# Kernel optimization log

Measured on AMD Instinct MI355X. Metric: run time of the kernel, lower is better.

## Reference

```python
import jax, jax.numpy as jnp
import numpy as np

NBINS = 256  # skimage threshold_otsu default


def _otsu_threshold(x):
    """Global Otsu threshold over the whole array, matching skimage.filters.threshold_otsu."""
    counts, edges = jnp.histogram(x.reshape(-1), bins=NBINS)
    counts = counts.astype(jnp.float32)
    centers = 0.5 * (edges[:-1] + edges[1:])  # [NBINS]

    # class probabilities / weights for all candidate thresholds
    w1 = jnp.cumsum(counts)                       # weight of class <= t
    w2 = jnp.cumsum(counts[::-1])[::-1]           # weight of class > t
    csum = jnp.cumsum(counts * centers)
    csum_rev = jnp.cumsum((counts * centers)[::-1])[::-1]
    m1 = csum / jnp.maximum(w1, 1.0)              # class means (guard empty bins)
    m2 = csum_rev / jnp.maximum(w2, 1.0)

    # between-class variance at each split point
    var12 = w1[:-1] * w2[1:] * (m1[:-1] - m2[1:]) ** 2  # [NBINS-1]
    idx = jnp.argmax(var12)
    return centers[idx]


def setup_inputs() -> dict:
    key = jax.random.key(0)
    inputs = jax.random.normal(key, (16, 1024, 2048, 1), dtype=jnp.float32)
    return {"inputs": inputs}


def reference(inputs) -> jnp.ndarray:
    x = inputs.astype(jnp.float32)
    thresh = _otsu_threshold(x)
    # ((image > thresh) * 1).astype(float32)
    return (x > thresh).astype(jnp.float32)
```

## Files before the change

kernel.cpp:

```cpp
#include <hip/hip_runtime.h>
#include <stdint.h>

#define NBINS 256
#define NCOPY 32

__device__ __forceinline__ uint32_t f2mono(float f) {
    uint32_t u = __float_as_uint(f);
    return (u & 0x80000000u) ? ~u : (u | 0x80000000u);
}
__device__ __forceinline__ float mono2f(uint32_t u) {
    uint32_t b = (u & 0x80000000u) ? (u & 0x7FFFFFFFu) : ~u;
    return __uint_as_float(b);
}

__device__ __forceinline__ float edge_at(int i, float minv, float delta) {
    return __fadd_rn(__fmul_rn((float)i, delta), minv);
}

__global__ void k_init(uint32_t* ws) {
    int i = threadIdx.x;
    if (i == 0) ws[0] = 0xFFFFFFFFu;
    if (i == 1) ws[1] = 0u;
    if (i == 2) ws[2] = 0u;
    if (i >= 4 && i < 4 + NBINS) ws[i] = 0u;
}

__device__ __forceinline__ float min4(float4 v) {
    return fminf(fminf(v.x, v.y), fminf(v.z, v.w));
}
__device__ __forceinline__ float max4(float4 v) {
    return fmaxf(fmaxf(v.x, v.y), fmaxf(v.z, v.w));
}

__global__ void __launch_bounds__(256) k_minmax(const float* __restrict__ in,
                                                int n, uint32_t* ws) {
    int tid = blockIdx.x * blockDim.x + threadIdx.x;
    int stride = gridDim.x * blockDim.x;
    int n4 = n >> 2;
    const float4* in4 = (const float4*)in;
    float vmin = INFINITY, vmax = -INFINITY;

    int i = tid;
    for (; i + 7 * stride < n4; i += 8 * stride) {
        float4 v0 = in4[i];
        float4 v1 = in4[i + stride];
        float4 v2 = in4[i + 2 * stride];
        float4 v3 = in4[i + 3 * stride];
        float4 v4 = in4[i + 4 * stride];
        float4 v5 = in4[i + 5 * stride];
        float4 v6 = in4[i + 6 * stride];
        float4 v7 = in4[i + 7 * stride];
        float mn0 = fminf(fminf(min4(v0), min4(v1)), fminf(min4(v2), min4(v3)));
        float mn1 = fminf(fminf(min4(v4), min4(v5)), fminf(min4(v6), min4(v7)));
        float mx0 = fmaxf(fmaxf(max4(v0), max4(v1)), fmaxf(max4(v2), max4(v3)));
        float mx1 = fmaxf(fmaxf(max4(v4), max4(v5)), fmaxf(max4(v6), max4(v7)));
        vmin = fminf(vmin, fminf(mn0, mn1));
        vmax = fmaxf(vmax, fmaxf(mx0, mx1));
    }
    for (; i < n4; i += stride) {
        float4 v = in4[i];
        vmin = fminf(vmin, min4(v));
        vmax = fmaxf(vmax, max4(v));
    }
    for (int j = (n4 << 2) + tid; j < n; j += stride) {
        float v = in[j];
        vmin = fminf(vmin, v);
        vmax = fmaxf(vmax, v);
    }
#pragma unroll
    for (int off = 32; off > 0; off >>= 1) {
        vmin = fminf(vmin, __shfl_down(vmin, off));
        vmax = fmaxf(vmax, __shfl_down(vmax, off));
    }
    __shared__ float smin[4], smax[4];
    int wave = threadIdx.x >> 6, lane = threadIdx.x & 63;
    if (lane == 0) { smin[wave] = vmin; smax[wave] = vmax; }
    __syncthreads();
    if (threadIdx.x == 0) {
        float m = smin[0], M = smax[0];
        for (int w = 1; w < 4; ++w) { m = fminf(m, smin[w]); M = fmaxf(M, smax[w]); }
        atomicMin(&ws[0], f2mono(m));
        atomicMax(&ws[1], f2mono(M));
    }
}

__device__ __forceinline__ int bin_of(float v, float minv, float invd) {
    float t = (v - minv) * invd;
    t = fminf(fmaxf(t, 0.0f), 255.0f);
    return (int)t;
}

__global__ void __launch_bounds__(256) k_hist(const float* __restrict__ in,
                                              int n, uint32_t* ws) {
    __shared__ uint32_t h[NBINS * NCOPY];
    for (int i = threadIdx.x; i < NBINS * NCOPY; i += blockDim.x) h[i] = 0;
    __syncthreads();
    float minv = mono2f(ws[0]);
    float maxv = mono2f(ws[1]);
    float invd = __fdiv_rn(256.0f, __fsub_rn(maxv, minv));
    int c = threadIdx.x & (NCOPY - 1);

    int tid = blockIdx.x * blockDim.x + threadIdx.x;
    int stride = gridDim.x * blockDim.x;
    int n4 = n >> 2;
    const float4* in4 = (const float4*)in;
    int i = tid;
    for (; i + 3 * stride < n4; i += 4 * stride) {
        float4 q0 = in4[i];
        float4 q1 = in4[i + stride];
        float4 q2 = in4[i + 2 * stride];
        float4 q3 = in4[i + 3 * stride];
        atomicAdd(&h[bin_of(q0.x, minv, invd) * NCOPY + c], 1u);
        atomicAdd(&h[bin_of(q0.y, minv, invd) * NCOPY + c], 1u);
        atomicAdd(&h[bin_of(q0.z, minv, invd) * NCOPY + c], 1u);
        atomicAdd(&h[bin_of(q0.w, minv, invd) * NCOPY + c], 1u);
        atomicAdd(&h[bin_of(q1.x, minv, invd) * NCOPY + c], 1u);
        atomicAdd(&h[bin_of(q1.y, minv, invd) * NCOPY + c], 1u);
        atomicAdd(&h[bin_of(q1.z, minv, invd) * NCOPY + c], 1u);
        atomicAdd(&h[bin_of(q1.w, minv, invd) * NCOPY + c], 1u);
        atomicAdd(&h[bin_of(q2.x, minv, invd) * NCOPY + c], 1u);
        atomicAdd(&h[bin_of(q2.y, minv, invd) * NCOPY + c], 1u);
        atomicAdd(&h[bin_of(q2.z, minv, invd) * NCOPY + c], 1u);
        atomicAdd(&h[bin_of(q2.w, minv, invd) * NCOPY + c], 1u);
        atomicAdd(&h[bin_of(q3.x, minv, invd) * NCOPY + c], 1u);
        atomicAdd(&h[bin_of(q3.y, minv, invd) * NCOPY + c], 1u);
        atomicAdd(&h[bin_of(q3.z, minv, invd) * NCOPY + c], 1u);
        atomicAdd(&h[bin_of(q3.w, minv, invd) * NCOPY + c], 1u);
    }
    for (; i < n4; i += stride) {
        float4 q = in4[i];
        atomicAdd(&h[bin_of(q.x, minv, invd) * NCOPY + c], 1u);
        atomicAdd(&h[bin_of(q.y, minv, invd) * NCOPY + c], 1u);
        atomicAdd(&h[bin_of(q.z, minv, invd) * NCOPY + c], 1u);
        atomicAdd(&h[bin_of(q.w, minv, invd) * NCOPY + c], 1u);
    }
    for (int j = (n4 << 2) + tid; j < n; j += stride) {
        atomicAdd(&h[bin_of(in[j], minv, invd) * NCOPY + c], 1u);
    }
    __syncthreads();
    for (int b = threadIdx.x; b < NBINS; b += blockDim.x) {
        uint32_t s = 0;
#pragma unroll
        for (int k = 0; k < NCOPY; ++k) s += h[b * NCOPY + k];
        if (s) atomicAdd(&ws[4 + b], s);
    }
}

__global__ void k_otsu(uint32_t* ws) {
    __shared__ float cnt[NBINS], ctr[NBINS], w1[NBINS], w2[NBINS],
                     cs[NBINS], csr[NBINS], scan[NBINS];
    int i = threadIdx.x;
    float minv = mono2f(ws[0]);
    float maxv = mono2f(ws[1]);
    float delta = __fdiv_rn(__fsub_rn(maxv, minv), 256.0f);

    cnt[i] = (float)ws[4 + i];
    float e0 = edge_at(i, minv, delta);
    float e1 = edge_at(i + 1, minv, delta);
    ctr[i] = __fmul_rn(0.5f, __fadd_rn(e0, e1));
    __syncthreads();

    scan[i] = cnt[i]; __syncthreads();
    for (int off = 1; off < NBINS; off <<= 1) {
        float v = scan[i];
        if (i >= off) v = __fadd_rn(scan[i - off], v);
        __syncthreads(); scan[i] = v; __syncthreads();
    }
    w1[i] = scan[i]; __syncthreads();

    scan[i] = __fmul_rn(cnt[i], ctr[i]); __syncthreads();
    for (int off = 1; off < NBINS; off <<= 1) {
        float v = scan[i];
        if (i >= off) v = __fadd_rn(scan[i - off], v);
        __syncthreads(); scan[i] = v; __syncthreads();
    }
    cs[i] = scan[i]; __syncthreads();

    scan[i] = cnt[i]; __syncthreads();
    for (int off = 1; off < NBINS; off <<= 1) {
        float v = scan[i];
        if (i + off < NBINS) v = __fadd_rn(v, scan[i + off]);
        __syncthreads(); scan[i] = v; __syncthreads();
    }
    w2[i] = scan[i]; __syncthreads();

    scan[i] = __fmul_rn(cnt[i], ctr[i]); __syncthreads();
    for (int off = 1; off < NBINS; off <<= 1) {
        float v = scan[i];
        if (i + off < NBINS) v = __fadd_rn(v, scan[i + off]);
        __syncthreads(); scan[i] = v; __syncthreads();
    }
    csr[i] = scan[i]; __syncthreads();

    if (i < NBINS - 1) {
        float m1 = __fdiv_rn(cs[i], fmaxf(w1[i], 1.0f));
        float m2 = __fdiv_rn(csr[i + 1], fmaxf(w2[i + 1], 1.0f));
        float d = __fsub_rn(m1, m2);
        float sq = __fmul_rn(d, d);
        scan[i] = __fmul_rn(__fmul_rn(w1[i], w2[i + 1]), sq);
    }
    __syncthreads();
    if (i == 0) {
        int best = 0; float bv = scan[0];
        for (int k = 1; k < NBINS - 1; ++k) {
            float v = scan[k];
            if (v > bv) { bv = v; best = k; }
        }
        ws[2] = __float_as_uint(ctr[best]);
    }
}

__global__ void __launch_bounds__(256) k_bin(const float* __restrict__ in,
                                             float* __restrict__ out,
                                             int n, const uint32_t* __restrict__ ws) {
    float t = __uint_as_float(ws[2]);
    int tid = blockIdx.x * blockDim.x + threadIdx.x;
    int stride = gridDim.x * blockDim.x;
    int n4 = n >> 2;
    const float4* in4 = (const float4*)in;
    float4* out4 = (float4*)out;
    int i = tid;
    for (; i + 3 * stride < n4; i += 4 * stride) {
        float4 v0 = in4[i];
        float4 v1 = in4[i + stride];
        float4 v2 = in4[i + 2 * stride];
        float4 v3 = in4[i + 3 * stride];
        float4 r0, r1, r2, r3;
        r0.x = v0.x > t ? 1.0f : 0.0f; r0.y = v0.y > t ? 1.0f : 0.0f;
        r0.z = v0.z > t ? 1.0f : 0.0f; r0.w = v0.w > t ? 1.0f : 0.0f;
        r1.x = v1.x > t ? 1.0f : 0.0f; r1.y = v1.y > t ? 1.0f : 0.0f;
        r1.z = v1.z > t ? 1.0f : 0.0f; r1.w = v1.w > t ? 1.0f : 0.0f;
        r2.x = v2.x > t ? 1.0f : 0.0f; r2.y = v2.y > t ? 1.0f : 0.0f;
        r2.z = v2.z > t ? 1.0f : 0.0f; r2.w = v2.w > t ? 1.0f : 0.0f;
        r3.x = v3.x > t ? 1.0f : 0.0f; r3.y = v3.y > t ? 1.0f : 0.0f;
        r3.z = v3.z > t ? 1.0f : 0.0f; r3.w = v3.w > t ? 1.0f : 0.0f;
        out4[i] = r0;
        out4[i + stride] = r1;
        out4[i + 2 * stride] = r2;
        out4[i + 3 * stride] = r3;
    }
    for (; i < n4; i += stride) {
        float4 v = in4[i];
        float4 r;
        r.x = v.x > t ? 1.0f : 0.0f;
        r.y = v.y > t ? 1.0f : 0.0f;
        r.z = v.z > t ? 1.0f : 0.0f;
        r.w = v.w > t ? 1.0f : 0.0f;
        out4[i] = r;
    }
    for (int j = (n4 << 2) + tid; j < n; j += stride) {
        out[j] = in[j] > t ? 1.0f : 0.0f;
    }
}

extern "C" void kernel_launch(void* const* d_in, const int* in_sizes, int n_in,
                              void* d_out, int out_size, void* d_ws, size_t ws_size,
                              hipStream_t stream) {
    const float* in = (const float*)d_in[0];
    float* out = (float*)d_out;
    uint32_t* ws = (uint32_t*)d_ws;
    int n = in_sizes[0];

    const int threads = 256;
    const int blocks = 2048;
    const int hist_blocks = 1280;

    hipLaunchKernelGGL(k_init, dim3(1), dim3(512), 0, stream, ws);
    hipLaunchKernelGGL(k_minmax, dim3(blocks), dim3(threads), 0, stream, in, n, ws);
    hipLaunchKernelGGL(k_hist, dim3(hist_blocks), dim3(threads), 0, stream, in, n, ws);
    hipLaunchKernelGGL(k_otsu, dim3(1), dim3(NBINS), 0, stream, ws);
    hipLaunchKernelGGL(k_bin, dim3(blocks), dim3(threads), 0, stream, in, out, n, ws);
}
```

Baseline: 169.8 us.

## Fuse minmax, histogram, Otsu and threshold into one persistent kernel with grid barriers

Replaces four separate kernel launches with a single persistent kernel of 1024 co-resident blocks. Phases are separated by software grid barriers built on agent-scope atomics. Block 0 computes the Otsu threshold between barriers. This removes inter-kernel launch gaps and tail effects. It adds spin-wait barrier cost and relies on all blocks being resident at once, or the kernel deadlocks until the spin-count escape triggers.

```diff
diff --git a/kernel.cpp b/kernel.cpp
--- a/kernel.cpp
+++ b/kernel.cpp
@@ -3,6 +3,9 @@
 
 #define NBINS 256
 #define NCOPY 32
+#define GRID_BLKS 1024
+#define TPB 256
+#define BAR0 320
 
 __device__ __forceinline__ uint32_t f2mono(float f) {
     uint32_t u = __float_as_uint(f);
@@ -15,6 +18,37 @@
 
 __device__ __forceinline__ float edge_at(int i, float minv, float delta) {
     return __fadd_rn(__fmul_rn((float)i, delta), minv);
+}
+
+__device__ __forceinline__ float min4(float4 v) {
+    return fminf(fminf(v.x, v.y), fminf(v.z, v.w));
+}
+__device__ __forceinline__ float max4(float4 v) {
+    return fmaxf(fmaxf(v.x, v.y), fmaxf(v.z, v.w));
+}
+
+__device__ __forceinline__ int bin_of(float v, float minv, float invd) {
+    float t = (v - minv) * invd;
+    t = fminf(fmaxf(t, 0.0f), 255.0f);
+    return (int)t;
+}
+
+__device__ __forceinline__ uint32_t aload(const uint32_t* p) {
+    return __hip_atomic_load(p, __ATOMIC_RELAXED, __HIP_MEMORY_SCOPE_AGENT);
+}
+
+__device__ __forceinline__ void grid_barrier(uint32_t* bar, uint32_t expect) {
+    __syncthreads();
+    if (threadIdx.x == 0) {
+        __threadfence();
+        __hip_atomic_fetch_add(bar, 1u, __ATOMIC_RELEASE, __HIP_MEMORY_SCOPE_AGENT);
+        uint32_t spins = 0;
+        while (__hip_atomic_load(bar, __ATOMIC_ACQUIRE, __HIP_MEMORY_SCOPE_AGENT) < expect) {
+            __builtin_amdgcn_s_sleep(8);
+            if (++spins > 100000000u) break;
+        }
+    }
+    __syncthreads();
 }
 
 __global__ void k_init(uint32_t* ws) {
@@ -23,233 +57,224 @@
     if (i == 1) ws[1] = 0u;
     if (i == 2) ws[2] = 0u;
     if (i >= 4 && i < 4 + NBINS) ws[i] = 0u;
-}
-
-__device__ __forceinline__ float min4(float4 v) {
-    return fminf(fminf(v.x, v.y), fminf(v.z, v.w));
-}
-__device__ __forceinline__ float max4(float4 v) {
-    return fmaxf(fmaxf(v.x, v.y), fmaxf(v.z, v.w));
-}
-
-__global__ void __launch_bounds__(256) k_minmax(const float* __restrict__ in,
-                                                int n, uint32_t* ws) {
-    int tid = blockIdx.x * blockDim.x + threadIdx.x;
-    int stride = gridDim.x * blockDim.x;
-    int n4 = n >> 2;
+    if (i >= BAR0 && i < BAR0 + 4) ws[i] = 0u;
+}
+
+__global__ void __launch_bounds__(TPB, 4) k_fused(const float* __restrict__ in,
+                                                  float* __restrict__ out,
+                                                  int n, uint32_t* ws) {
+    __shared__ uint32_t h[NBINS * NCOPY];
+    float* sf = (float*)h;
+
+    const int gtid = blockIdx.x * blockDim.x + threadIdx.x;
+    const int gstride = gridDim.x * blockDim.x;
+    const int wave = threadIdx.x >> 6, lane = threadIdx.x & 63;
+    const int n4 = n >> 2;
     const float4* in4 = (const float4*)in;
-    float vmin = INFINITY, vmax = -INFINITY;
-
-    int i = tid;
-    for (; i + 7 * stride < n4; i += 8 * stride) {
-        float4 v0 = in4[i];
-        float4 v1 = in4[i + stride];
-        float4 v2 = in4[i + 2 * stride];
-        float4 v3 = in4[i + 3 * stride];
-        float4 v4 = in4[i + 4 * stride];
-        float4 v5 = in4[i + 5 * stride];
-        float4 v6 = in4[i + 6 * stride];
-        float4 v7 = in4[i + 7 * stride];
-        float mn0 = fminf(fminf(min4(v0), min4(v1)), fminf(min4(v2), min4(v3)));
-        float mn1 = fminf(fminf(min4(v4), min4(v5)), fminf(min4(v6), min4(v7)));
-        float mx0 = fmaxf(fmaxf(max4(v0), max4(v1)), fmaxf(max4(v2), max4(v3)));
-        float mx1 = fmaxf(fmaxf(max4(v4), max4(v5)), fmaxf(max4(v6), max4(v7)));
-        vmin = fminf(vmin, fminf(mn0, mn1));
-        vmax = fmaxf(vmax, fmaxf(mx0, mx1));
-    }
-    for (; i < n4; i += stride) {
-        float4 v = in4[i];
-        vmin = fminf(vmin, min4(v));
-        vmax = fmaxf(vmax, max4(v));
-    }
-    for (int j = (n4 << 2) + tid; j < n; j += stride) {
-        float v = in[j];
-        vmin = fminf(vmin, v);
-        vmax = fmaxf(vmax, v);
-    }
+    const uint32_t expect = gridDim.x;
+
+    {
+        float vmin = INFINITY, vmax = -INFINITY;
+        int i = gtid;
+        for (; i + 7 * gstride < n4; i += 8 * gstride) {
+            float4 v0 = in4[i];
+            float4 v1 = in4[i + gstride];
+            float4 v2 = in4[i + 2 * gstride];
+            float4 v3 = in4[i + 3 * gstride];
+            float4 v4 = in4[i + 4 * gstride];
+            float4 v5 = in4[i + 5 * gstride];
+            float4 v6 = in4[i + 6 * gstride];
+            float4 v7 = in4[i + 7 * gstride];
+            float mn0 = fminf(fminf(min4(v0), min4(v1)), fminf(min4(v2), min4(v3)));
+            float mn1 = fminf(fminf(min4(v4), min4(v5)), fminf(min4(v6), min4(v7)));
+            float mx0 = fmaxf(fmaxf(max4(v0), max4(v1)), fmaxf(max4(v2), max4(v3)));
+            float mx1 = fmaxf(fmaxf(max4(v4), max4(v5)), fmaxf(max4(v6), max4(v7)));
+            vmin = fminf(vmin, fminf(mn0, mn1));
+            vmax = fmaxf(vmax, fmaxf(mx0, mx1));
+        }
+        for (; i < n4; i += gstride) {
+            float4 v = in4[i];
+            vmin = fminf(vmin, min4(v));
+            vmax = fmaxf(vmax, max4(v));
+        }
+        for (int j = (n4 << 2) + gtid; j < n; j += gstride) {
+            float v = in[j];
+            vmin = fminf(vmin, v);
+            vmax = fmaxf(vmax, v);
+        }
 #pragma unroll
-    for (int off = 32; off > 0; off >>= 1) {
-        vmin = fminf(vmin, __shfl_down(vmin, off));
-        vmax = fmaxf(vmax, __shfl_down(vmax, off));
-    }
-    __shared__ float smin[4], smax[4];
-    int wave = threadIdx.x >> 6, lane = threadIdx.x & 63;
-    if (lane == 0) { smin[wave] = vmin; smax[wave] = vmax; }
-    __syncthreads();
-    if (threadIdx.x == 0) {
-        float m = smin[0], M = smax[0];
-        for (int w = 1; w < 4; ++w) { m = fminf(m, smin[w]); M = fmaxf(M, smax[w]); }
-        atomicMin(&ws[0], f2mono(m));
-        atomicMax(&ws[1], f2mono(M));
-    }
-}
-
-__device__ __forceinline__ int bin_of(float v, float minv, float invd) {
-    float t = (v - minv) * invd;
-    t = fminf(fmaxf(t, 0.0f), 255.0f);
-    return (int)t;
-}
-
-__global__ void __launch_bounds__(256) k_hist(const float* __restrict__ in,
-                                              int n, uint32_t* ws) {
-    __shared__ uint32_t h[NBINS * NCOPY];
-    for (int i = threadIdx.x; i < NBINS * NCOPY; i += blockDim.x) h[i] = 0;
-    __syncthreads();
-    float minv = mono2f(ws[0]);
-    float maxv = mono2f(ws[1]);
-    float invd = __fdiv_rn(256.0f, __fsub_rn(maxv, minv));
-    int c = threadIdx.x & (NCOPY - 1);
-
-    int tid = blockIdx.x * blockDim.x + threadIdx.x;
-    int stride = gridDim.x * blockDim.x;
-    int n4 = n >> 2;
-    const float4* in4 = (const float4*)in;
-    int i = tid;
-    for (; i + 3 * stride < n4; i += 4 * stride) {
-        float4 q0 = in4[i];
-        float4 q1 = in4[i + stride];
-        float4 q2 = in4[i + 2 * stride];
-        float4 q3 = in4[i + 3 * stride];
-        atomicAdd(&h[bin_of(q0.x, minv, invd) * NCOPY + c], 1u);
-        atomicAdd(&h[bin_of(q0.y, minv, invd) * NCOPY + c], 1u);
-        atomicAdd(&h[bin_of(q0.z, minv, invd) * NCOPY + c], 1u);
-        atomicAdd(&h[bin_of(q0.w, minv, invd) * NCOPY + c], 1u);
-        atomicAdd(&h[bin_of(q1.x, minv, invd) * NCOPY + c], 1u);
-        atomicAdd(&h[bin_of(q1.y, minv, invd) * NCOPY + c], 1u);
-        atomicAdd(&h[bin_of(q1.z, minv, invd) * NCOPY + c], 1u);
-        atomicAdd(&h[bin_of(q1.w, minv, invd) * NCOPY + c], 1u);
-        atomicAdd(&h[bin_of(q2.x, minv, invd) * NCOPY + c], 1u);
-        atomicAdd(&h[bin_of(q2.y, minv, invd) * NCOPY + c], 1u);
-        atomicAdd(&h[bin_of(q2.z, minv, invd) * NCOPY + c], 1u);
-        atomicAdd(&h[bin_of(q2.w, minv, invd) * NCOPY + c], 1u);
-        atomicAdd(&h[bin_of(q3.x, minv, invd) * NCOPY + c], 1u);
-        atomicAdd(&h[bin_of(q3.y, minv, invd) * NCOPY + c], 1u);
-        atomicAdd(&h[bin_of(q3.z, minv, invd) * NCOPY + c], 1u);
-        atomicAdd(&h[bin_of(q3.w, minv, invd) * NCOPY + c], 1u);
-    }
-    for (; i < n4; i += stride) {
-        float4 q = in4[i];
-        atomicAdd(&h[bin_of(q.x, minv, invd) * NCOPY + c], 1u);
-        atomicAdd(&h[bin_of(q.y, minv, invd) * NCOPY + c], 1u);
-        atomicAdd(&h[bin_of(q.z, minv, invd) * NCOPY + c], 1u);
-        atomicAdd(&h[bin_of(q.w, minv, invd) * NCOPY + c], 1u);
-    }
-    for (int j = (n4 << 2) + tid; j < n; j += stride) {
-        atomicAdd(&h[bin_of(in[j], minv, invd) * NCOPY + c], 1u);
-    }
-    __syncthreads();
-    for (int b = threadIdx.x; b < NBINS; b += blockDim.x) {
-        uint32_t s = 0;
+        for (int off = 32; off > 0; off >>= 1) {
+            vmin = fminf(vmin, __shfl_down(vmin, off));
+            vmax = fmaxf(vmax, __shfl_down(vmax, off));
+        }
+        if (lane == 0) { sf[wave] = vmin; sf[8 + wave] = vmax; }
+        __syncthreads();
+        if (threadIdx.x == 0) {
+            float m = sf[0], M = sf[8];
+            for (int w = 1; w < 4; ++w) { m = fminf(m, sf[w]); M = fmaxf(M, sf[8 + w]); }
+            atomicMin(&ws[0], f2mono(m));
+            atomicMax(&ws[1], f2mono(M));
+        }
+    }
+    grid_barrier(&ws[BAR0 + 0], expect);
+
+    {
+        float minv = mono2f(aload(&ws[0]));
+        float maxv = mono2f(aload(&ws[1]));
+        float invd = __fdiv_rn(256.0f, __fsub_rn(maxv, minv));
+        int c = threadIdx.x & (NCOPY - 1);
+        for (int i = threadIdx.x; i < NBINS * NCOPY; i += blockDim.x) h[i] = 0;
+        __syncthreads();
+
+        int i = gtid;
+        for (; i + 3 * gstride < n4; i += 4 * gstride) {
+            float4 q0 = in4[i];
+            float4 q1 = in4[i + gstride];
+            float4 q2 = in4[i + 2 * gstride];
+            float4 q3 = in4[i + 3 * gstride];
+            atomicAdd(&h[bin_of(q0.x, minv, invd) * NCOPY + c], 1u);
+            atomicAdd(&h[bin_of(q0.y, minv, invd) * NCOPY + c], 1u);
+            atomicAdd(&h[bin_of(q0.z, minv, invd) * NCOPY + c], 1u);
+            atomicAdd(&h[bin_of(q0.w, minv, invd) * NCOPY + c], 1u);
+            atomicAdd(&h[bin_of(q1.x, minv, invd) * NCOPY + c], 1u);
+            atomicAdd(&h[bin_of(q1.y, minv, invd) * NCOPY + c], 1u);
+            atomicAdd(&h[bin_of(q1.z, minv, invd) * NCOPY + c], 1u);
+            atomicAdd(&h[bin_of(q1.w, minv, invd) * NCOPY + c], 1u);
+            atomicAdd(&h[bin_of(q2.x, minv, invd) * NCOPY + c], 1u);
+            atomicAdd(&h[bin_of(q2.y, minv, invd) * NCOPY + c], 1u);
+            atomicAdd(&h[bin_of(q2.z, minv, invd) * NCOPY + c], 1u);
+            atomicAdd(&h[bin_of(q2.w, minv, invd) * NCOPY + c], 1u);
+            atomicAdd(&h[bin_of(q3.x, minv, invd) * NCOPY + c], 1u);
+            atomicAdd(&h[bin_of(q3.y, minv, invd) * NCOPY + c], 1u);
+            atomicAdd(&h[bin_of(q3.z, minv, invd) * NCOPY + c], 1u);
+            atomicAdd(&h[bin_of(q3.w, minv, invd) * NCOPY + c], 1u);
+        }
+        for (; i < n4; i += gstride) {
+            float4 q = in4[i];
+            atomicAdd(&h[bin_of(q.x, minv, invd) * NCOPY + c], 1u);
+            atomicAdd(&h[bin_of(q.y, minv, invd) * NCOPY + c], 1u);
+            atomicAdd(&h[bin_of(q.z, minv, invd) * NCOPY + c], 1u);
+            atomicAdd(&h[bin_of(q.w, minv, invd) * NCOPY + c], 1u);
+        }
+        for (int j = (n4 << 2) + gtid; j < n; j += gstride) {
+            atomicAdd(&h[bin_of(in[j], minv, invd) * NCOPY + c], 1u);
+        }
+        __syncthreads();
+        for (int b = threadIdx.x; b < NBINS; b += blockDim.x) {
+            uint32_t s = 0;
 #pragma unroll
-        for (int k = 0; k < NCOPY; ++k) s += h[b * NCOPY + k];
-        if (s) atomicAdd(&ws[4 + b], s);
-    }
-}
-
-__global__ void k_otsu(uint32_t* ws) {
-    __shared__ float cnt[NBINS], ctr[NBINS], w1[NBINS], w2[NBINS],
-                     cs[NBINS], csr[NBINS], scan[NBINS];
-    int i = threadIdx.x;
-    float minv = mono2f(ws[0]);
-    float maxv = mono2f(ws[1]);
-    float delta = __fdiv_rn(__fsub_rn(maxv, minv), 256.0f);
-
-    cnt[i] = (float)ws[4 + i];
-    float e0 = edge_at(i, minv, delta);
-    float e1 = edge_at(i + 1, minv, delta);
-    ctr[i] = __fmul_rn(0.5f, __fadd_rn(e0, e1));
-    __syncthreads();
-
-    scan[i] = cnt[i]; __syncthreads();
-    for (int off = 1; off < NBINS; off <<= 1) {
-        float v = scan[i];
-        if (i >= off) v = __fadd_rn(scan[i - off], v);
-        __syncthreads(); scan[i] = v; __syncthreads();
-    }
-    w1[i] = scan[i]; __syncthreads();
-
-    scan[i] = __fmul_rn(cnt[i], ctr[i]); __syncthreads();
-    for (int off = 1; off < NBINS; off <<= 1) {
-        float v = scan[i];
-        if (i >= off) v = __fadd_rn(scan[i - off], v);
-        __syncthreads(); scan[i] = v; __syncthreads();
-    }
-    cs[i] = scan[i]; __syncthreads();
-
-    scan[i] = cnt[i]; __syncthreads();
-    for (int off = 1; off < NBINS; off <<= 1) {
-        float v = scan[i];
-        if (i + off < NBINS) v = __fadd_rn(v, scan[i + off]);
-        __syncthreads(); scan[i] = v; __syncthreads();
-    }
-    w2[i] = scan[i]; __syncthreads();
-
-    scan[i] = __fmul_rn(cnt[i], ctr[i]); __syncthreads();
-    for (int off = 1; off < NBINS; off <<= 1) {
-        float v = scan[i];
-        if (i + off < NBINS) v = __fadd_rn(v, scan[i + off]);
-        __syncthreads(); scan[i] = v; __syncthreads();
-    }
-    csr[i] = scan[i]; __syncthreads();
-
-    if (i < NBINS - 1) {
-        float m1 = __fdiv_rn(cs[i], fmaxf(w1[i], 1.0f));
-        float m2 = __fdiv_rn(csr[i + 1], fmaxf(w2[i + 1], 1.0f));
-        float d = __fsub_rn(m1, m2);
-        float sq = __fmul_rn(d, d);
-        scan[i] = __fmul_rn(__fmul_rn(w1[i], w2[i + 1]), sq);
-    }
-    __syncthreads();
-    if (i == 0) {
-        int best = 0; float bv = scan[0];
-        for (int k = 1; k < NBINS - 1; ++k) {
-            float v = scan[k];
-            if (v > bv) { bv = v; best = k; }
-        }
-        ws[2] = __float_as_uint(ctr[best]);
-    }
-}
-
-__global__ void __launch_bounds__(256) k_bin(const float* __restrict__ in,
-                                             float* __restrict__ out,
-                                             int n, const uint32_t* __restrict__ ws) {
-    float t = __uint_as_float(ws[2]);
-    int tid = blockIdx.x * blockDim.x + threadIdx.x;
-    int stride = gridDim.x * blockDim.x;
-    int n4 = n >> 2;
-    const float4* in4 = (const float4*)in;
-    float4* out4 = (float4*)out;
-    int i = tid;
-    for (; i + 3 * stride < n4; i += 4 * stride) {
-        float4 v0 = in4[i];
-        float4 v1 = in4[i + stride];
-        float4 v2 = in4[i + 2 * stride];
-        float4 v3 = in4[i + 3 * stride];
-        float4 r0, r1, r2, r3;
-        r0.x = v0.x > t ? 1.0f : 0.0f; r0.y = v0.y > t ? 1.0f : 0.0f;
-        r0.z = v0.z > t ? 1.0f : 0.0f; r0.w = v0.w > t ? 1.0f : 0.0f;
-        r1.x = v1.x > t ? 1.0f : 0.0f; r1.y = v1.y > t ? 1.0f : 0.0f;
-        r1.z = v1.z > t ? 1.0f : 0.0f; r1.w = v1.w > t ? 1.0f : 0.0f;
-        r2.x = v2.x > t ? 1.0f : 0.0f; r2.y = v2.y > t ? 1.0f : 0.0f;
-        r2.z = v2.z > t ? 1.0f : 0.0f; r2.w = v2.w > t ? 1.0f : 0.0f;
-        r3.x = v3.x > t ? 1.0f : 0.0f; r3.y = v3.y > t ? 1.0f : 0.0f;
-        r3.z = v3.z > t ? 1.0f : 0.0f; r3.w = v3.w > t ? 1.0f : 0.0f;
-        out4[i] = r0;
-        out4[i + stride] = r1;
-        out4[i + 2 * stride] = r2;
-        out4[i + 3 * stride] = r3;
-    }
-    for (; i < n4; i += stride) {
-        float4 v = in4[i];
-        float4 r;
-        r.x = v.x > t ? 1.0f : 0.0f;
-        r.y = v.y > t ? 1.0f : 0.0f;
-        r.z = v.z > t ? 1.0f : 0.0f;
-        r.w = v.w > t ? 1.0f : 0.0f;
-        out4[i] = r;
-    }
-    for (int j = (n4 << 2) + tid; j < n; j += stride) {
-        out[j] = in[j] > t ? 1.0f : 0.0f;
+            for (int k = 0; k < NCOPY; ++k) s += h[b * NCOPY + k];
+            if (s) atomicAdd(&ws[4 + b], s);
+        }
+    }
+    grid_barrier(&ws[BAR0 + 1], expect);
+
+    if (blockIdx.x == 0) {
+        float* cnt = sf;
+        float* ctr = sf + NBINS;
+        float* w1 = sf + 2 * NBINS;
+        float* w2 = sf + 3 * NBINS;
+        float* cs = sf + 4 * NBINS;
+        float* csr = sf + 5 * NBINS;
+        float* scan = sf + 6 * NBINS;
+        int i = threadIdx.x;
+        float minv = mono2f(aload(&ws[0]));
+        float maxv = mono2f(aload(&ws[1]));
+        float delta = __fdiv_rn(__fsub_rn(maxv, minv), 256.0f);
+
+        cnt[i] = (float)aload(&ws[4 + i]);
+        float e0 = edge_at(i, minv, delta);
+        float e1 = edge_at(i + 1, minv, delta);
+        ctr[i] = __fmul_rn(0.5f, __fadd_rn(e0, e1));
+        __syncthreads();
+
+        scan[i] = cnt[i]; __syncthreads();
+        for (int off = 1; off < NBINS; off <<= 1) {
+            float v = scan[i];
+            if (i >= off) v = __fadd_rn(scan[i - off], v);
+            __syncthreads(); scan[i] = v; __syncthreads();
+        }
+        w1[i] = scan[i]; __syncthreads();
+
+        scan[i] = __fmul_rn(cnt[i], ctr[i]); __syncthreads();
+        for (int off = 1; off < NBINS; off <<= 1) {
+            float v = scan[i];
+            if (i >= off) v = __fadd_rn(scan[i - off], v);
+            __syncthreads(); scan[i] = v; __syncthreads();
+        }
+        cs[i] = scan[i]; __syncthreads();
+
+        scan[i] = cnt[i]; __syncthreads();
+        for (int off = 1; off < NBINS; off <<= 1) {
+            float v = scan[i];
+            if (i + off < NBINS) v = __fadd_rn(v, scan[i + off]);
+            __syncthreads(); scan[i] = v; __syncthreads();
+        }
+        w2[i] = scan[i]; __syncthreads();
+
+        scan[i] = __fmul_rn(cnt[i], ctr[i]); __syncthreads();
+        for (int off = 1; off < NBINS; off <<= 1) {
+            float v = scan[i];
+            if (i + off < NBINS) v = __fadd_rn(v, scan[i + off]);
+            __syncthreads(); scan[i] = v; __syncthreads();
+        }
+        csr[i] = scan[i]; __syncthreads();
+
+        if (i < NBINS - 1) {
+            float m1 = __fdiv_rn(cs[i], fmaxf(w1[i], 1.0f));
+            float m2 = __fdiv_rn(csr[i + 1], fmaxf(w2[i + 1], 1.0f));
+            float d = __fsub_rn(m1, m2);
+            float sq = __fmul_rn(d, d);
+            scan[i] = __fmul_rn(__fmul_rn(w1[i], w2[i + 1]), sq);
+        }
+        __syncthreads();
+        if (i == 0) {
+            int best = 0; float bv = scan[0];
+            for (int k = 1; k < NBINS - 1; ++k) {
+                float v = scan[k];
+                if (v > bv) { bv = v; best = k; }
+            }
+            __hip_atomic_store(&ws[2], __float_as_uint(ctr[best]),
+                               __ATOMIC_RELEASE, __HIP_MEMORY_SCOPE_AGENT);
+        }
+    }
+    grid_barrier(&ws[BAR0 + 2], expect);
+
+    {
+        float t = __uint_as_float(aload(&ws[2]));
+        float4* out4 = (float4*)out;
+        int i = gtid;
+        for (; i + 3 * gstride < n4; i += 4 * gstride) {
+            float4 v0 = in4[i];
+            float4 v1 = in4[i + gstride];
+            float4 v2 = in4[i + 2 * gstride];
+            float4 v3 = in4[i + 3 * gstride];
+            float4 r0, r1, r2, r3;
+            r0.x = v0.x > t ? 1.0f : 0.0f; r0.y = v0.y > t ? 1.0f : 0.0f;
+            r0.z = v0.z > t ? 1.0f : 0.0f; r0.w = v0.w > t ? 1.0f : 0.0f;
+            r1.x = v1.x > t ? 1.0f : 0.0f; r1.y = v1.y > t ? 1.0f : 0.0f;
+            r1.z = v1.z > t ? 1.0f : 0.0f; r1.w = v1.w > t ? 1.0f : 0.0f;
+            r2.x = v2.x > t ? 1.0f : 0.0f; r2.y = v2.y > t ? 1.0f : 0.0f;
+            r2.z = v2.z > t ? 1.0f : 0.0f; r2.w = v2.w > t ? 1.0f : 0.0f;
+            r3.x = v3.x > t ? 1.0f : 0.0f; r3.y = v3.y > t ? 1.0f : 0.0f;
+            r3.z = v3.z > t ? 1.0f : 0.0f; r3.w = v3.w > t ? 1.0f : 0.0f;
+            out4[i] = r0;
+            out4[i + gstride] = r1;
+            out4[i + 2 * gstride] = r2;
+            out4[i + 3 * gstride] = r3;
+        }
+        for (; i < n4; i += gstride) {
+            float4 v = in4[i];
+            float4 r;
+            r.x = v.x > t ? 1.0f : 0.0f;
+            r.y = v.y > t ? 1.0f : 0.0f;
+            r.z = v.z > t ? 1.0f : 0.0f;
+            r.w = v.w > t ? 1.0f : 0.0f;
+            out4[i] = r;
+        }
+        for (int j = (n4 << 2) + gtid; j < n; j += gstride) {
+            out[j] = in[j] > t ? 1.0f : 0.0f;
+        }
     }
 }
 
@@ -261,13 +286,7 @@
     uint32_t* ws = (uint32_t*)d_ws;
     int n = in_sizes[0];
 
-    const int threads = 256;
-    const int blocks = 2048;
-    const int hist_blocks = 1280;
-
     hipLaunchKernelGGL(k_init, dim3(1), dim3(512), 0, stream, ws);
-    hipLaunchKernelGGL(k_minmax, dim3(blocks), dim3(threads), 0, stream, in, n, ws);
-    hipLaunchKernelGGL(k_hist, dim3(hist_blocks), dim3(threads), 0, stream, in, n, ws);
-    hipLaunchKernelGGL(k_otsu, dim3(1), dim3(NBINS), 0, stream, ws);
-    hipLaunchKernelGGL(k_bin, dim3(blocks), dim3(threads), 0, stream, in, out, n, ws);
-}
+    hipLaunchKernelGGL(k_fused, dim3(GRID_BLKS), dim3(TPB), 0, stream,
+                       in, out, n, ws);
+}
```

New measurement: 458.8 us. 2.7x slower.

## Fuse Otsu threshold computation into last histogram block via completion counter

Applied to the files above, without the earlier changes.

The separate single-block Otsu kernel is removed. Each histogram block now increments a global counter, and the last block to finish computes the prefix scans and argmax in its own shared memory. This saves one kernel launch and the gap between launches, at the cost of an extra atomic and threadfence per block. The binarize kernel's unroll is also cut from four float4 loads per iteration to two.

```diff
diff --git a/kernel.cpp b/kernel.cpp
--- a/kernel.cpp
+++ b/kernel.cpp
@@ -3,6 +3,7 @@
 
 #define NBINS 256
 #define NCOPY 32
+#define HIST_BLOCKS 1280
 
 __device__ __forceinline__ uint32_t f2mono(float f) {
     uint32_t u = __float_as_uint(f);
@@ -22,6 +23,7 @@
     if (i == 0) ws[0] = 0xFFFFFFFFu;
     if (i == 1) ws[1] = 0u;
     if (i == 2) ws[2] = 0u;
+    if (i == 3) ws[3] = 0u;
     if (i >= 4 && i < 4 + NBINS) ws[i] = 0u;
 }
 
@@ -144,69 +146,86 @@
         for (int k = 0; k < NCOPY; ++k) s += h[b * NCOPY + k];
         if (s) atomicAdd(&ws[4 + b], s);
     }
-}
-
-__global__ void k_otsu(uint32_t* ws) {
-    __shared__ float cnt[NBINS], ctr[NBINS], w1[NBINS], w2[NBINS],
-                     cs[NBINS], csr[NBINS], scan[NBINS];
-    int i = threadIdx.x;
-    float minv = mono2f(ws[0]);
-    float maxv = mono2f(ws[1]);
-    float delta = __fdiv_rn(__fsub_rn(maxv, minv), 256.0f);
-
-    cnt[i] = (float)ws[4 + i];
-    float e0 = edge_at(i, minv, delta);
-    float e1 = edge_at(i + 1, minv, delta);
-    ctr[i] = __fmul_rn(0.5f, __fadd_rn(e0, e1));
-    __syncthreads();
-
-    scan[i] = cnt[i]; __syncthreads();
-    for (int off = 1; off < NBINS; off <<= 1) {
-        float v = scan[i];
-        if (i >= off) v = __fadd_rn(scan[i - off], v);
-        __syncthreads(); scan[i] = v; __syncthreads();
-    }
-    w1[i] = scan[i]; __syncthreads();
-
-    scan[i] = __fmul_rn(cnt[i], ctr[i]); __syncthreads();
-    for (int off = 1; off < NBINS; off <<= 1) {
-        float v = scan[i];
-        if (i >= off) v = __fadd_rn(scan[i - off], v);
-        __syncthreads(); scan[i] = v; __syncthreads();
-    }
-    cs[i] = scan[i]; __syncthreads();
-
-    scan[i] = cnt[i]; __syncthreads();
-    for (int off = 1; off < NBINS; off <<= 1) {
-        float v = scan[i];
-        if (i + off < NBINS) v = __fadd_rn(v, scan[i + off]);
-        __syncthreads(); scan[i] = v; __syncthreads();
-    }
-    w2[i] = scan[i]; __syncthreads();
-
-    scan[i] = __fmul_rn(cnt[i], ctr[i]); __syncthreads();
-    for (int off = 1; off < NBINS; off <<= 1) {
-        float v = scan[i];
-        if (i + off < NBINS) v = __fadd_rn(v, scan[i + off]);
-        __syncthreads(); scan[i] = v; __syncthreads();
-    }
-    csr[i] = scan[i]; __syncthreads();
-
-    if (i < NBINS - 1) {
-        float m1 = __fdiv_rn(cs[i], fmaxf(w1[i], 1.0f));
-        float m2 = __fdiv_rn(csr[i + 1], fmaxf(w2[i + 1], 1.0f));
-        float d = __fsub_rn(m1, m2);
-        float sq = __fmul_rn(d, d);
-        scan[i] = __fmul_rn(__fmul_rn(w1[i], w2[i + 1]), sq);
-    }
-    __syncthreads();
-    if (i == 0) {
-        int best = 0; float bv = scan[0];
-        for (int k = 1; k < NBINS - 1; ++k) {
-            float v = scan[k];
-            if (v > bv) { bv = v; best = k; }
-        }
-        ws[2] = __float_as_uint(ctr[best]);
+
+    __shared__ int amLast;
+    __threadfence();
+    if (threadIdx.x == 0) {
+        uint32_t t = atomicAdd(&ws[3], 1u);
+        amLast = (t == (uint32_t)(gridDim.x - 1)) ? 1 : 0;
+    }
+    __syncthreads();
+    if (!amLast) return;
+    __threadfence();
+
+    {
+        float* sf = (float*)h;
+        float* cnt = sf;
+        float* ctr = sf + NBINS;
+        float* w1 = sf + 2 * NBINS;
+        float* w2 = sf + 3 * NBINS;
+        float* cs = sf + 4 * NBINS;
+        float* csr = sf + 5 * NBINS;
+        float* scan = sf + 6 * NBINS;
+        int i = threadIdx.x;
+        float delta = __fdiv_rn(__fsub_rn(maxv, minv), 256.0f);
+
+        __syncthreads();
+        cnt[i] = (float)__hip_atomic_load(&ws[4 + i], __ATOMIC_RELAXED,
+                                          __HIP_MEMORY_SCOPE_AGENT);
+        float e0 = edge_at(i, minv, delta);
+        float e1 = edge_at(i + 1, minv, delta);
+        ctr[i] = __fmul_rn(0.5f, __fadd_rn(e0, e1));
+        __syncthreads();
+
+        scan[i] = cnt[i]; __syncthreads();
+        for (int off = 1; off < NBINS; off <<= 1) {
+            float v = scan[i];
+            if (i >= off) v = __fadd_rn(scan[i - off], v);
+            __syncthreads(); scan[i] = v; __syncthreads();
+        }
+        w1[i] = scan[i]; __syncthreads();
+
+        scan[i] = __fmul_rn(cnt[i], ctr[i]); __syncthreads();
+        for (int off = 1; off < NBINS; off <<= 1) {
+            float v = scan[i];
+            if (i >= off) v = __fadd_rn(scan[i - off], v);
+            __syncthreads(); scan[i] = v; __syncthreads();
+        }
+        cs[i] = scan[i]; __syncthreads();
+
+        scan[i] = cnt[i]; __syncthreads();
+        for (int off = 1; off < NBINS; off <<= 1) {
+            float v = scan[i];
+            if (i + off < NBINS) v = __fadd_rn(v, scan[i + off]);
+            __syncthreads(); scan[i] = v; __syncthreads();
+        }
+        w2[i] = scan[i]; __syncthreads();
+
+        scan[i] = __fmul_rn(cnt[i], ctr[i]); __syncthreads();
+        for (int off = 1; off < NBINS; off <<= 1) {
+            float v = scan[i];
+            if (i + off < NBINS) v = __fadd_rn(v, scan[i + off]);
+            __syncthreads(); scan[i] = v; __syncthreads();
+        }
+        csr[i] = scan[i]; __syncthreads();
+
+        if (i < NBINS - 1) {
+            float m1 = __fdiv_rn(cs[i], fmaxf(w1[i], 1.0f));
+            float m2 = __fdiv_rn(csr[i + 1], fmaxf(w2[i + 1], 1.0f));
+            float d = __fsub_rn(m1, m2);
+            float sq = __fmul_rn(d, d);
+            scan[i] = __fmul_rn(__fmul_rn(w1[i], w2[i + 1]), sq);
+        }
+        __syncthreads();
+        if (i == 0) {
+            int best = 0; float bv = scan[0];
+            for (int k = 1; k < NBINS - 1; ++k) {
+                float v = scan[k];
+                if (v > bv) { bv = v; best = k; }
+            }
+            __hip_atomic_store(&ws[2], __float_as_uint(ctr[best]),
+                               __ATOMIC_RELEASE, __HIP_MEMORY_SCOPE_AGENT);
+        }
     }
 }
 
@@ -220,24 +239,16 @@
     const float4* in4 = (const float4*)in;
     float4* out4 = (float4*)out;
     int i = tid;
-    for (; i + 3 * stride < n4; i += 4 * stride) {
+    for (; i + stride < n4; i += 2 * stride) {
         float4 v0 = in4[i];
         float4 v1 = in4[i + stride];
-        float4 v2 = in4[i + 2 * stride];
-        float4 v3 = in4[i + 3 * stride];
-        float4 r0, r1, r2, r3;
+        float4 r0, r1;
         r0.x = v0.x > t ? 1.0f : 0.0f; r0.y = v0.y > t ? 1.0f : 0.0f;
         r0.z = v0.z > t ? 1.0f : 0.0f; r0.w = v0.w > t ? 1.0f : 0.0f;
         r1.x = v1.x > t ? 1.0f : 0.0f; r1.y = v1.y > t ? 1.0f : 0.0f;
         r1.z = v1.z > t ? 1.0f : 0.0f; r1.w = v1.w > t ? 1.0f : 0.0f;
-        r2.x = v2.x > t ? 1.0f : 0.0f; r2.y = v2.y > t ? 1.0f : 0.0f;
-        r2.z = v2.z > t ? 1.0f : 0.0f; r2.w = v2.w > t ? 1.0f : 0.0f;
-        r3.x = v3.x > t ? 1.0f : 0.0f; r3.y = v3.y > t ? 1.0f : 0.0f;
-        r3.z = v3.z > t ? 1.0f : 0.0f; r3.w = v3.w > t ? 1.0f : 0.0f;
         out4[i] = r0;
         out4[i + stride] = r1;
-        out4[i + 2 * stride] = r2;
-        out4[i + 3 * stride] = r3;
     }
     for (; i < n4; i += stride) {
         float4 v = in4[i];
@@ -263,11 +274,9 @@
 
     const int threads = 256;
     const int blocks = 2048;
-    const int hist_blocks = 1280;
 
     hipLaunchKernelGGL(k_init, dim3(1), dim3(512), 0, stream, ws);
     hipLaunchKernelGGL(k_minmax, dim3(blocks), dim3(threads), 0, stream, in, n, ws);
-    hipLaunchKernelGGL(k_hist, dim3(hist_blocks), dim3(threads), 0, stream, in, n, ws);
-    hipLaunchKernelGGL(k_otsu, dim3(1), dim3(NBINS), 0, stream, ws);
+    hipLaunchKernelGGL(k_hist, dim3(HIST_BLOCKS), dim3(threads), 0, stream, in, n, ws);
     hipLaunchKernelGGL(k_bin, dim3(blocks), dim3(threads), 0, stream, in, out, n, ws);
 }
```

After: 217.4 us. +28.0%, slower.

## Fold Otsu threshold computation into binarize kernel and retune histogram kernel

Applied to the files above, without the earlier changes.

Removes the separate single-block Otsu kernel launch by having every block of the binarize kernel recompute the threshold redundantly from the global histogram in shared memory. The histogram kernel switches to 16 private copies per bin, 8-way unrolled float4 loads, launch bounds for 8 blocks per CU, and 2048 blocks. This removes one launch and its serialization gap, but every one of the 2048 binarize blocks now runs four barrier-heavy scans before streaming, and halving the private copies may increase shared-atomic contention.

```diff
diff --git a/kernel.cpp b/kernel.cpp
--- a/kernel.cpp
+++ b/kernel.cpp
@@ -2,7 +2,7 @@
 #include <stdint.h>
 
 #define NBINS 256
-#define NCOPY 32
+#define NCOPY 16
 
 __device__ __forceinline__ uint32_t f2mono(float f) {
     uint32_t u = __float_as_uint(f);
@@ -90,8 +90,16 @@
     return (int)t;
 }
 
-__global__ void __launch_bounds__(256) k_hist(const float* __restrict__ in,
-                                              int n, uint32_t* ws) {
+__device__ __forceinline__ void hist4(float4 q, float minv, float invd,
+                                      uint32_t* h, int c) {
+    atomicAdd(&h[bin_of(q.x, minv, invd) * NCOPY + c], 1u);
+    atomicAdd(&h[bin_of(q.y, minv, invd) * NCOPY + c], 1u);
+    atomicAdd(&h[bin_of(q.z, minv, invd) * NCOPY + c], 1u);
+    atomicAdd(&h[bin_of(q.w, minv, invd) * NCOPY + c], 1u);
+}
+
+__global__ void __launch_bounds__(256, 8) k_hist(const float* __restrict__ in,
+                                                 int n, uint32_t* ws) {
     __shared__ uint32_t h[NBINS * NCOPY];
     for (int i = threadIdx.x; i < NBINS * NCOPY; i += blockDim.x) h[i] = 0;
     __syncthreads();
@@ -105,34 +113,27 @@
     int n4 = n >> 2;
     const float4* in4 = (const float4*)in;
     int i = tid;
-    for (; i + 3 * stride < n4; i += 4 * stride) {
+    for (; i + 7 * stride < n4; i += 8 * stride) {
         float4 q0 = in4[i];
         float4 q1 = in4[i + stride];
         float4 q2 = in4[i + 2 * stride];
         float4 q3 = in4[i + 3 * stride];
-        atomicAdd(&h[bin_of(q0.x, minv, invd) * NCOPY + c], 1u);
-        atomicAdd(&h[bin_of(q0.y, minv, invd) * NCOPY + c], 1u);
-        atomicAdd(&h[bin_of(q0.z, minv, invd) * NCOPY + c], 1u);
-        atomicAdd(&h[bin_of(q0.w, minv, invd) * NCOPY + c], 1u);
-        atomicAdd(&h[bin_of(q1.x, minv, invd) * NCOPY + c], 1u);
-        atomicAdd(&h[bin_of(q1.y, minv, invd) * NCOPY + c], 1u);
-        atomicAdd(&h[bin_of(q1.z, minv, invd) * NCOPY + c], 1u);
-        atomicAdd(&h[bin_of(q1.w, minv, invd) * NCOPY + c], 1u);
-        atomicAdd(&h[bin_of(q2.x, minv, invd) * NCOPY + c], 1u);
-        atomicAdd(&h[bin_of(q2.y, minv, invd) * NCOPY + c], 1u);
-        atomicAdd(&h[bin_of(q2.z, minv, invd) * NCOPY + c], 1u);
-        atomicAdd(&h[bin_of(q2.w, minv, invd) * NCOPY + c], 1u);
-        atomicAdd(&h[bin_of(q3.x, minv, invd) * NCOPY + c], 1u);
-        atomicAdd(&h[bin_of(q3.y, minv, invd) * NCOPY + c], 1u);
-        atomicAdd(&h[bin_of(q3.z, minv, invd) * NCOPY + c], 1u);
-        atomicAdd(&h[bin_of(q3.w, minv, invd) * NCOPY + c], 1u);
+        float4 q4 = in4[i + 4 * stride];
+        float4 q5 = in4[i + 5 * stride];
+        float4 q6 = in4[i + 6 * stride];
+        float4 q7 = in4[i + 7 * stride];
+        hist4(q0, minv, invd, h, c);
+        hist4(q1, minv, invd, h, c);
+        hist4(q2, minv, invd, h, c);
+        hist4(q3, minv, invd, h, c);
+        hist4(q4, minv, invd, h, c);
+        hist4(q5, minv, invd, h, c);
+        hist4(q6, minv, invd, h, c);
+        hist4(q7, minv, invd, h, c);
     }
     for (; i < n4; i += stride) {
         float4 q = in4[i];
-        atomicAdd(&h[bin_of(q.x, minv, invd) * NCOPY + c], 1u);
-        atomicAdd(&h[bin_of(q.y, minv, invd) * NCOPY + c], 1u);
-        atomicAdd(&h[bin_of(q.z, minv, invd) * NCOPY + c], 1u);
-        atomicAdd(&h[bin_of(q.w, minv, invd) * NCOPY + c], 1u);
+        hist4(q, minv, invd, h, c);
     }
     for (int j = (n4 << 2) + tid; j < n; j += stride) {
         atomicAdd(&h[bin_of(in[j], minv, invd) * NCOPY + c], 1u);
@@ -146,74 +147,75 @@
     }
 }
 
-__global__ void k_otsu(uint32_t* ws) {
-    __shared__ float cnt[NBINS], ctr[NBINS], w1[NBINS], w2[NBINS],
-                     cs[NBINS], csr[NBINS], scan[NBINS];
-    int i = threadIdx.x;
-    float minv = mono2f(ws[0]);
-    float maxv = mono2f(ws[1]);
-    float delta = __fdiv_rn(__fsub_rn(maxv, minv), 256.0f);
-
-    cnt[i] = (float)ws[4 + i];
-    float e0 = edge_at(i, minv, delta);
-    float e1 = edge_at(i + 1, minv, delta);
-    ctr[i] = __fmul_rn(0.5f, __fadd_rn(e0, e1));
-    __syncthreads();
-
-    scan[i] = cnt[i]; __syncthreads();
-    for (int off = 1; off < NBINS; off <<= 1) {
-        float v = scan[i];
-        if (i >= off) v = __fadd_rn(scan[i - off], v);
-        __syncthreads(); scan[i] = v; __syncthreads();
-    }
-    w1[i] = scan[i]; __syncthreads();
-
-    scan[i] = __fmul_rn(cnt[i], ctr[i]); __syncthreads();
-    for (int off = 1; off < NBINS; off <<= 1) {
-        float v = scan[i];
-        if (i >= off) v = __fadd_rn(scan[i - off], v);
-        __syncthreads(); scan[i] = v; __syncthreads();
-    }
-    cs[i] = scan[i]; __syncthreads();
-
-    scan[i] = cnt[i]; __syncthreads();
-    for (int off = 1; off < NBINS; off <<= 1) {
-        float v = scan[i];
-        if (i + off < NBINS) v = __fadd_rn(v, scan[i + off]);
-        __syncthreads(); scan[i] = v; __syncthreads();
-    }
-    w2[i] = scan[i]; __syncthreads();
-
-    scan[i] = __fmul_rn(cnt[i], ctr[i]); __syncthreads();
-    for (int off = 1; off < NBINS; off <<= 1) {
-        float v = scan[i];
-        if (i + off < NBINS) v = __fadd_rn(v, scan[i + off]);
-        __syncthreads(); scan[i] = v; __syncthreads();
-    }
-    csr[i] = scan[i]; __syncthreads();
-
-    if (i < NBINS - 1) {
-        float m1 = __fdiv_rn(cs[i], fmaxf(w1[i], 1.0f));
-        float m2 = __fdiv_rn(csr[i + 1], fmaxf(w2[i + 1], 1.0f));
-        float d = __fsub_rn(m1, m2);
-        float sq = __fmul_rn(d, d);
-        scan[i] = __fmul_rn(__fmul_rn(w1[i], w2[i + 1]), sq);
-    }
-    __syncthreads();
-    if (i == 0) {
-        int best = 0; float bv = scan[0];
-        for (int k = 1; k < NBINS - 1; ++k) {
-            float v = scan[k];
-            if (v > bv) { bv = v; best = k; }
-        }
-        ws[2] = __float_as_uint(ctr[best]);
-    }
-}
-
 __global__ void __launch_bounds__(256) k_bin(const float* __restrict__ in,
                                              float* __restrict__ out,
                                              int n, const uint32_t* __restrict__ ws) {
-    float t = __uint_as_float(ws[2]);
+    __shared__ float cnt[NBINS], ctr[NBINS], w1[NBINS], w2[NBINS],
+                     cs[NBINS], csr[NBINS], scan[NBINS], tsh[1];
+    {
+        int i = threadIdx.x;
+        float minv = mono2f(ws[0]);
+        float maxv = mono2f(ws[1]);
+        float delta = __fdiv_rn(__fsub_rn(maxv, minv), 256.0f);
+
+        cnt[i] = (float)ws[4 + i];
+        float e0 = edge_at(i, minv, delta);
+        float e1 = edge_at(i + 1, minv, delta);
+        ctr[i] = __fmul_rn(0.5f, __fadd_rn(e0, e1));
+        __syncthreads();
+
+        scan[i] = cnt[i]; __syncthreads();
+        for (int off = 1; off < NBINS; off <<= 1) {
+            float v = scan[i];
+            if (i >= off) v = __fadd_rn(scan[i - off], v);
+            __syncthreads(); scan[i] = v; __syncthreads();
+        }
+        w1[i] = scan[i]; __syncthreads();
+
+        scan[i] = __fmul_rn(cnt[i], ctr[i]); __syncthreads();
+        for (int off = 1; off < NBINS; off <<= 1) {
+            float v = scan[i];
+            if (i >= off) v = __fadd_rn(scan[i - off], v);
+            __syncthreads(); scan[i] = v; __syncthreads();
+        }
+        cs[i] = scan[i]; __syncthreads();
+
+        scan[i] = cnt[i]; __syncthreads();
+        for (int off = 1; off < NBINS; off <<= 1) {
+            float v = scan[i];
+            if (i + off < NBINS) v = __fadd_rn(v, scan[i + off]);
+            __syncthreads(); scan[i] = v; __syncthreads();
+        }
+        w2[i] = scan[i]; __syncthreads();
+
+        scan[i] = __fmul_rn(cnt[i], ctr[i]); __syncthreads();
+        for (int off = 1; off < NBINS; off <<= 1) {
+            float v = scan[i];
+            if (i + off < NBINS) v = __fadd_rn(v, scan[i + off]);
+            __syncthreads(); scan[i] = v; __syncthreads();
+        }
+        csr[i] = scan[i]; __syncthreads();
+
+        if (i < NBINS - 1) {
+            float m1 = __fdiv_rn(cs[i], fmaxf(w1[i], 1.0f));
+            float m2 = __fdiv_rn(csr[i + 1], fmaxf(w2[i + 1], 1.0f));
+            float d = __fsub_rn(m1, m2);
+            float sq = __fmul_rn(d, d);
+            scan[i] = __fmul_rn(__fmul_rn(w1[i], w2[i + 1]), sq);
+        }
+        __syncthreads();
+        if (i == 0) {
+            int best = 0; float bv = scan[0];
+            for (int k = 1; k < NBINS - 1; ++k) {
+                float v = scan[k];
+                if (v > bv) { bv = v; best = k; }
+            }
+            tsh[0] = ctr[best];
+        }
+        __syncthreads();
+    }
+    float t = tsh[0];
+
     int tid = blockIdx.x * blockDim.x + threadIdx.x;
     int stride = gridDim.x * blockDim.x;
     int n4 = n >> 2;
@@ -263,11 +265,9 @@
 
     const int threads = 256;
     const int blocks = 2048;
-    const int hist_blocks = 1280;
 
     hipLaunchKernelGGL(k_init, dim3(1), dim3(512), 0, stream, ws);
     hipLaunchKernelGGL(k_minmax, dim3(blocks), dim3(threads), 0, stream, in, n, ws);
-    hipLaunchKernelGGL(k_hist, dim3(hist_blocks), dim3(threads), 0, stream, in, n, ws);
-    hipLaunchKernelGGL(k_otsu, dim3(1), dim3(NBINS), 0, stream, ws);
+    hipLaunchKernelGGL(k_hist, dim3(blocks), dim3(threads), 0, stream, in, n, ws);
     hipLaunchKernelGGL(k_bin, dim3(blocks), dim3(threads), 0, stream, in, out, n, ws);
 }
```

New measurement: 183.8 us. 8.2% more time.
